# Kernel optimization log

Hardware: AMD Instinct MI355X
Metric: run time of the kernel (lower is better)

## Reference

```python
import jax, jax.numpy as jnp
import numpy as np

B, K, T, D, NH, HD, DFF, L = 2, 512, 2048, 1024, 16, 64, 4096, 2
EPS = 1e-5


def rotate_half(x):
    x1, x2 = jnp.split(x, 2, axis=-1)
    return jnp.concatenate([-x2, x1], axis=-1)


def rmsnorm(x, w):
    return x * jax.lax.rsqrt(jnp.mean(x * x, axis=-1, keepdims=True) + EPS) * w


def setup_inputs():
    key = jax.random.key(0)
    ks = jax.random.split(key, 16)
    x_processed = jax.random.normal(ks[0], (B, K, D), jnp.float32)
    # counts[b] = number of chunks n; boundaries[b, :n-1] = ascending chunk ends in (0, T),
    # positions >= n-1 padded with T (sentinel, never used by the original loop).
    counts = jax.random.randint(ks[1], (B,), K // 2, K + 1)
    raw = jnp.sort(jax.random.randint(ks[2], (B, K), 1, T), axis=1)
    j = jnp.arange(K)[None, :]
    boundaries = jnp.where(j < counts[:, None] - 1, raw, T)
    x_residual = jax.random.normal(ks[3], (B, T, D), jnp.float32)
    inv_freq = 1.0 / (10000.0 ** (jnp.arange(0, HD, 2, dtype=jnp.float32) / HD))
    freqs = jnp.arange(T, dtype=jnp.float32)[:, None] * inv_freq[None, :]  # [T, HD//2]
    emb = jnp.concatenate([freqs, freqs], axis=-1)                          # [T, HD]
    cos, sin = jnp.cos(emb), jnp.sin(emb)
    s = 0.02
    wq = jax.random.normal(ks[4], (L, D, D), jnp.float32) * s
    wk = jax.random.normal(ks[5], (L, D, D), jnp.float32) * s
    wv = jax.random.normal(ks[6], (L, D, D), jnp.float32) * s
    wo = jax.random.normal(ks[7], (L, D, D), jnp.float32) * s
    w1 = jax.random.normal(ks[8], (L, D, DFF), jnp.float32) * s
    w3 = jax.random.normal(ks[9], (L, D, DFF), jnp.float32) * s
    w2 = jax.random.normal(ks[10], (L, DFF, D), jnp.float32) * s
    attn_norm_w = jnp.ones((L, D), jnp.float32)
    mlp_norm_w = jnp.ones((L, D), jnp.float32)
    final_norm_w = jnp.ones((D,), jnp.float32)
    return {"x_processed": x_processed, "boundaries": boundaries, "counts": counts,
            "x_residual": x_residual, "cos": cos, "sin": sin, "seq_len": T,
            "wq": wq, "wk": wk, "wv": wv, "wo": wo,
            "attn_norm_w": attn_norm_w, "mlp_norm_w": mlp_norm_w,
            "w1": w1, "w3": w3, "w2": w2, "final_norm_w": final_norm_w}


def reference(x_processed, boundaries, counts, x_residual, cos, sin, seq_len,
              wq, wk, wv, wo, attn_norm_w, mlp_norm_w, w1, w3, w2, final_norm_w):
    Bn, Kn, Dn = x_processed.shape
    Tn = x_residual.shape[1]
    # Vectorized chunk expansion: token t belongs to chunk i = #{boundaries <= t}
    # (boundaries ascending; entries beyond n-1 are padded with seq_len so they never count).
    t = jnp.arange(Tn)
    idx = jax.vmap(lambda row: jnp.searchsorted(row, t, side='right'))(boundaries)  # [B, T]
    x = jnp.take_along_axis(x_processed, idx[:, :, None], axis=1) + x_residual     # [B, T, D]

    mask = jnp.tril(jnp.ones((Tn, Tn), dtype=bool))
    scale = 1.0 / jnp.sqrt(jnp.float32(HD))
    c = cos[None, :, None, :]
    s = sin[None, :, None, :]
    for l in range(L):
        h = rmsnorm(x, attn_norm_w[l])
        q = (h @ wq[l]).reshape(Bn, Tn, NH, HD)
        k = (h @ wk[l]).reshape(Bn, Tn, NH, HD)
        v = (h @ wv[l]).reshape(Bn, Tn, NH, HD)
        q = q * c + rotate_half(q) * s
        k = k * c + rotate_half(k) * s
        scores = jnp.einsum('bthd,bshd->bhts', q, k) * scale
        scores = jnp.where(mask[None, None], scores, -jnp.inf)
        probs = jax.nn.softmax(scores, axis=-1)
        o = jnp.einsum('bhts,bshd->bthd', probs, v).reshape(Bn, Tn, Dn)
        x = x + o @ wo[l]
        h = rmsnorm(x, mlp_norm_w[l])
        x = x + (jax.nn.silu(h @ w1[l]) * (h @ w3[l])) @ w2[l]
    return rmsnorm(x, final_norm_w)
```

## Files before the change

### kernel.cpp

```cpp
#include <hip/hip_runtime.h>
#include <stdint.h>

typedef __attribute__((ext_vector_type(8))) short s16x8;
typedef __attribute__((ext_vector_type(4))) float f32x4;

#define CB 2
#define CT 2048
#define CD 1024
#define CNH 16
#define CHD 64
#define CDFF 4096
#define CKB 512

__device__ __forceinline__ short f2bf(float f){
  union { float f; uint32_t u; } v; v.f = f;
  uint32_t r = v.u + 0x7FFFu + ((v.u >> 16) & 1u);
  return (short)(r >> 16);
}
__device__ __forceinline__ float bf2f(short h){
  union { uint32_t u; float f; } v; v.u = ((uint32_t)(uint16_t)h) << 16;
  return v.f;
}
__device__ __forceinline__ uint32_t cvtpk_bf16(float lo, float hi){
  uint32_t r;
  asm("v_cvt_pk_bf16_f32 %0, %1, %2" : "=v"(r) : "v"(lo), "v"(hi));
  return r;
}

#define GLOAD16(g, l) __builtin_amdgcn_global_load_lds( \
    (const __attribute__((address_space(1))) void*)(g), \
    (__attribute__((address_space(3))) void*)(l), 16, 0, 0)

__global__ void gather_rms_kernel(const float* __restrict__ xp, const int* __restrict__ bnd,
                                  const float* __restrict__ xr, const float* __restrict__ w,
                                  float* __restrict__ x, short* __restrict__ hbuf){
  int row = blockIdx.x;
  int b = row >> 11, t = row & 2047;
  int tid = threadIdx.x;
  int lo = 0, hi = CKB;
  while (lo < hi){ int mid = (lo + hi) >> 1; if (bnd[b*CKB + mid] <= t) lo = mid + 1; else hi = mid; }
  const float4 s  = ((const float4*)(xp + ((size_t)b*CKB + lo)*CD))[tid];
  const float4 rr = ((const float4*)(xr + (size_t)row*CD))[tid];
  float4 a; a.x = s.x + rr.x; a.y = s.y + rr.y; a.z = s.z + rr.z; a.w = s.w + rr.w;
  ((float4*)(x + (size_t)row*CD))[tid] = a;
  float ss = a.x*a.x + a.y*a.y + a.z*a.z + a.w*a.w;
  #pragma unroll
  for (int m = 1; m < 64; m <<= 1) ss += __shfl_xor(ss, m);
  __shared__ float red[4];
  if ((tid & 63) == 0) red[tid >> 6] = ss;
  __syncthreads();
  float tot = red[0] + red[1] + red[2] + red[3];
  float scale = rsqrtf(tot * (1.0f/1024.0f) + 1e-5f);
  const float4 wv = ((const float4*)w)[tid];
  short4 o;
  o.x = f2bf(a.x*scale*wv.x); o.y = f2bf(a.y*scale*wv.y);
  o.z = f2bf(a.z*scale*wv.z); o.w = f2bf(a.w*scale*wv.w);
  ((short4*)hbuf)[(size_t)row*256 + tid] = o;
}

__global__ void wtrans_qkvo_kernel(const float* __restrict__ wq, const float* __restrict__ wk,
                                   const float* __restrict__ wv, const float* __restrict__ wo,
                                   short* __restrict__ qkvT, short* __restrict__ woT){
  __shared__ __align__(16) float tile[64*65];
  const float* W; short* dst;
  const int z = blockIdx.z;
  if (z == 0){ W = wq; dst = qkvT; }
  else if (z == 1){ W = wk; dst = qkvT + (size_t)1024*1024; }
  else if (z == 2){ W = wv; dst = qkvT + (size_t)2048*1024; }
  else { W = wo; dst = woT; }
  int n0 = blockIdx.x*64, k0 = blockIdx.y*64;
  #pragma unroll
  for (int i = 0; i < 16; ++i){
    int e = threadIdx.x + 256*i; int kl = e >> 6, nl = e & 63;
    tile[kl*65 + nl] = W[(size_t)(k0 + kl)*1024 + n0 + nl];
  }
  __syncthreads();
  #pragma unroll
  for (int i = 0; i < 16; ++i){
    int e = threadIdx.x + 256*i; int nl = e >> 6, kl = e & 63;
    dst[(size_t)(n0 + nl)*1024 + k0 + kl] = f2bf(tile[kl*65 + nl]);
  }
}

__global__ void wtrans_kernel(const float* __restrict__ W, short* __restrict__ dst,
                              int Kd, int Nd){
  __shared__ __align__(16) float tile[64*65];
  int n0 = blockIdx.x*64, k0 = blockIdx.y*64;
  #pragma unroll
  for (int i = 0; i < 16; ++i){
    int e = threadIdx.x + 256*i; int kl = e >> 6, nl = e & 63;
    tile[kl*65 + nl] = W[(size_t)(k0 + kl)*Nd + n0 + nl];
  }
  __syncthreads();
  #pragma unroll
  for (int i = 0; i < 16; ++i){
    int e = threadIdx.x + 256*i; int nl = e >> 6, kl = e & 63;
    dst[(size_t)(n0 + nl)*Kd + k0 + kl] = f2bf(tile[kl*65 + nl]);
  }
}

__global__ void wtrans_inter2_kernel(const float* __restrict__ w1p, const float* __restrict__ w3p,
                                     short* __restrict__ dst){
  __shared__ __align__(16) float tile[64*65];
  const float* W = blockIdx.z ? w3p : w1p;
  const int off16 = blockIdx.z ? 16 : 0;
  int n0 = blockIdx.x*64, k0 = blockIdx.y*64;
  #pragma unroll
  for (int i = 0; i < 16; ++i){
    int e = threadIdx.x + 256*i; int kl = e >> 6, nl = e & 63;
    tile[kl*65 + nl] = W[(size_t)(k0 + kl)*4096 + n0 + nl];
  }
  __syncthreads();
  #pragma unroll
  for (int i = 0; i < 16; ++i){
    int e = threadIdx.x + 256*i; int nl = e >> 6, kl = e & 63;
    int c = n0 + nl;
    int frow = ((c >> 4) << 5) + off16 + (c & 15);
    dst[(size_t)frow*1024 + k0 + kl] = f2bf(tile[kl*65 + nl]);
  }
}

template<int OUT_BF16>
__global__ void redrms_kernel(float* __restrict__ x, const short* __restrict__ Cp,
                              const float* __restrict__ w, void* __restrict__ outv){
  int row = blockIdx.x, tid = threadIdx.x;
  size_t i = (size_t)row*256 + tid;
  const short4* p0 = (const short4*)Cp;
  const short4* p1 = p0 + (size_t)1048576;
  const short4* p2 = p1 + (size_t)1048576;
  const short4* p3 = p2 + (size_t)1048576;
  float4 a = ((float4*)x)[i];
  short4 q0 = p0[i], q1 = p1[i], q2 = p2[i], q3 = p3[i];
  a.x += (bf2f(q0.x) + bf2f(q1.x)) + (bf2f(q2.x) + bf2f(q3.x));
  a.y += (bf2f(q0.y) + bf2f(q1.y)) + (bf2f(q2.y) + bf2f(q3.y));
  a.z += (bf2f(q0.z) + bf2f(q1.z)) + (bf2f(q2.z) + bf2f(q3.z));
  a.w += (bf2f(q0.w) + bf2f(q1.w)) + (bf2f(q2.w) + bf2f(q3.w));
  if (OUT_BF16) ((float4*)x)[i] = a;
  float ss = a.x*a.x + a.y*a.y + a.z*a.z + a.w*a.w;
  #pragma unroll
  for (int m = 1; m < 64; m <<= 1) ss += __shfl_xor(ss, m);
  __shared__ float red[4];
  if ((tid & 63) == 0) red[tid >> 6] = ss;
  __syncthreads();
  float tot = red[0] + red[1] + red[2] + red[3];
  float scale = rsqrtf(tot * (1.0f/1024.0f) + 1e-5f);
  const float4 wv = ((const float4*)w)[tid];
  if (OUT_BF16){
    short4 o;
    o.x = f2bf(a.x*scale*wv.x); o.y = f2bf(a.y*scale*wv.y);
    o.z = f2bf(a.z*scale*wv.z); o.w = f2bf(a.w*scale*wv.w);
    ((short4*)outv)[(size_t)row*256 + tid] = o;
  } else {
    float4 o;
    o.x = a.x*scale*wv.x; o.y = a.y*scale*wv.y;
    o.z = a.z*scale*wv.z; o.w = a.w*scale*wv.w;
    ((float4*)outv)[(size_t)row*256 + tid] = o;
  }
}

__device__ __forceinline__ void swz_block_id(int id, int NX, int NY, int& bm, int& bn){
  const int nwg = NX*NY;
  const int qq = nwg >> 3, rr8 = nwg & 7;
  const int xcd = id & 7, loc = id >> 3;
  const int wgid = (xcd < rr8 ? xcd*(qq+1) : rr8*(qq+1) + (xcd-rr8)*qq) + loc;
  const int GM = 8;
  const int gsz = GM * NX;
  const int gidg = wgid / gsz;
  const int remg = wgid - gidg*gsz;
  bm = gidg*GM + (remg % GM);
  bn = remg / GM;
}

__global__ __launch_bounds__(256) void gemm_splitk(const short* __restrict__ A,
                                                   const short* __restrict__ Bt,
                                                   short* __restrict__ Cp,
                                                   int M, int N, int Ktot, int Kchunk,
                                                   int NX, int NY){
  __shared__ __align__(16) short sA[2][128*32];
  __shared__ __align__(16) short sB[2][128*32];
  const int tid = threadIdx.x;
  const int lane = tid & 63, wid = tid >> 6;
  const int wm = wid >> 1, wn = wid & 1;
  const int lr = lane & 15, lg = lane >> 4;
  const int nin = NX*NY;
  const int split = blockIdx.x / nin;
  const int inner = blockIdx.x - split*nin;
  int bm, bn; swz_block_id(inner, NX, NY, bm, bn);
  const int bm0 = bm * 128, bn0 = bn * 128;
  const int koff = split * Kchunk;

  f32x4 acc[4][4];
  #pragma unroll
  for (int i = 0; i < 4; ++i)
    #pragma unroll
    for (int j = 0; j < 4; ++j) acc[i][j] = (f32x4){0.f,0.f,0.f,0.f};

  const short* gA = A  + (size_t)(bm0 + wid*32 + (lane >> 2))*Ktot + koff + (lane & 3)*8;
  const short* gB = Bt + (size_t)(bn0 + wid*32 + (lane >> 2))*Ktot + koff + (lane & 3)*8;

  #pragma unroll
  for (int iss = 0; iss < 2; ++iss){
    GLOAD16(gA + (size_t)iss*16*Ktot, &sA[0][wid*1024 + iss*16*32]);
    GLOAD16(gB + (size_t)iss*16*Ktot, &sB[0][wid*1024 + iss*16*32]);
  }
  __syncthreads();

  int cur = 0;
  for (int k0 = 0; k0 < Kchunk; k0 += 32){
    if (k0 + 32 < Kchunk){
      #pragma unroll
      for (int iss = 0; iss < 2; ++iss){
        GLOAD16(gA + (size_t)iss*16*Ktot + k0 + 32, &sA[cur^1][wid*1024 + iss*16*32]);
        GLOAD16(gB + (size_t)iss*16*Ktot + k0 + 32, &sB[cur^1][wid*1024 + iss*16*32]);
      }
    }
    s16x8 af[4], bq[4];
    #pragma unroll
    for (int i = 0; i < 4; ++i) af[i] = *(const s16x8*)&sA[cur][(wm*64 + i*16 + lr)*32 + lg*8];
    #pragma unroll
    for (int j = 0; j < 4; ++j) bq[j] = *(const s16x8*)&sB[cur][(wn*64 + j*16 + lr)*32 + lg*8];
    #pragma unroll
    for (int i = 0; i < 4; ++i)
      #pragma unroll
      for (int j = 0; j < 4; ++j)
        acc[i][j] = __builtin_amdgcn_mfma_f32_16x16x32_bf16(af[i], bq[j], acc[i][j], 0, 0, 0);
    __syncthreads();
    cur ^= 1;
  }

  short* C = Cp + (size_t)split*M*N;
  #pragma unroll
  for (int i = 0; i < 4; ++i){
    int row0 = bm0 + wm*64 + i*16 + lg*4;
    #pragma unroll
    for (int j = 0; j < 4; ++j){
      int col = bn0 + wn*64 + j*16 + lr;
      #pragma unroll
      for (int r = 0; r < 4; ++r) C[(size_t)(row0 + r)*N + col] = f2bf(acc[i][j][r]);
    }
  }
}

#define STAGE8(u, kt, bufx) do { \
  const short* Gp_ = ((u)&1) ? Bt : A; \
  const int rb_ = ((u)&1) ? bn0 : bm0; \
  const int kh_ = (u)>>1; \
  _Pragma("unroll") \
  for (int L_ = 0; L_ < 2; ++L_){ \
    int rowS_ = L_*128 + wid*16 + (lane>>2); \
    int sp_ = (lane&3) ^ ((rowS_>>1)&3); \
    GLOAD16(Gp_ + (size_t)(rb_ + rowS_)*Kstr + (size_t)(kt)*64 + kh_*32 + sp_*8, \
            &sAB[bufx][u][(L_*512 + wid*64)*8]); \
  } \
} while(0)

#define LDSRD(bufx, u, rowv) \
  (*(const s16x8*)&sAB[bufx][u][(rowv)*32 + (((lg) ^ (((rowv)>>1)&3))<<3)])

template<int FUSE>
__global__ __launch_bounds__(512, 2) void gemm8p(const short* __restrict__ A,
                                                 const short* __restrict__ Bt,
                                                 void* __restrict__ Cv,
                                                 short* __restrict__ Qo,
                                                 short* __restrict__ Ko,
                                                 short* __restrict__ Vo,
                                                 const float* __restrict__ cosb,
                                                 const float* __restrict__ sinb,
                                                 int M, int N, int Kstr, int Kchunk,
                                                 int NX, int NY){
  __shared__ __align__(16) short sAB[2][4][256*32];
  const int tid = threadIdx.x;
  const int lane = tid & 63, wid = tid >> 6;
  const int wm = wid >> 2, wn = wid & 3;
  const int lr = lane & 15, lg = lane >> 4;
  const int nin = NX*NY;
  const int split = blockIdx.x / nin;
  const int inner = blockIdx.x - split*nin;
  int bm, bn; swz_block_id(inner, NX, NY, bm, bn);
  const int bm0 = bm * 256, bn0 = bn * 256;
  A  += (size_t)split * Kchunk;
  Bt += (size_t)split * Kchunk;

  f32x4 acc[8][4];
  #pragma unroll
  for (int i = 0; i < 8; ++i)
    #pragma unroll
    for (int j = 0; j < 4; ++j) acc[i][j] = (f32x4){0.f,0.f,0.f,0.f};

  const int NK = Kchunk >> 6;
  STAGE8(0, 0, 0); STAGE8(1, 0, 0); STAGE8(2, 0, 0); STAGE8(3, 0, 0);
  if (NK > 1){
    STAGE8(0, 1, 1); STAGE8(1, 1, 1); STAGE8(2, 1, 1);
    asm volatile("s_waitcnt vmcnt(10)" ::: "memory");
  } else {
    asm volatile("s_waitcnt vmcnt(4)" ::: "memory");
  }
  __builtin_amdgcn_s_barrier();

  s16x8 afp[8];
  #pragma unroll 1
  for (int kt = 0; kt < NK; ++kt){
    const int cur = kt & 1, nxt = cur ^ 1;
    const bool st1 = (kt + 1 < NK);
    const bool st2 = (kt + 2 < NK);

    if (st1) STAGE8(3, kt+1, nxt);
    {
      #pragma unroll
      for (int i_ = 0; i_ < 8; ++i_) afp[i_] = LDSRD(cur, 0, wm*128 + i_*16 + lr);
      s16x8 b0 = LDSRD(cur, 1, wn*64 + lr);
      s16x8 b1 = LDSRD(cur, 1, wn*64 + 16 + lr);
      __builtin_amdgcn_s_barrier();
      asm volatile("s_waitcnt lgkmcnt(0)" ::: "memory");
      __builtin_amdgcn_s_setprio(1);
      #pragma unroll
      for (int i_ = 0; i_ < 8; ++i_){
        acc[i_][0] = __builtin_amdgcn_mfma_f32_16x16x32_bf16(afp[i_], b0, acc[i_][0], 0, 0, 0);
        acc[i_][1] = __builtin_amdgcn_mfma_f32_16x16x32_bf16(afp[i_], b1, acc[i_][1], 0, 0, 0);
      }
      __builtin_amdgcn_s_setprio(0);
      __builtin_amdgcn_s_barrier();
    }
    if (st2) STAGE8(0, kt+2, cur);
    {
      s16x8 b2 = LDSRD(cur, 1, wn*64 + 32 + lr);
      s16x8 b3 = LDSRD(cur, 1, wn*64 + 48 + lr);
      __builtin_amdgcn_s_barrier();
      asm volatile("s_waitcnt lgkmcnt(0)" ::: "memory");
      __builtin_amdgcn_s_setprio(1);
      #pragma unroll
      for (int i_ = 0; i_ < 8; ++i_){
        acc[i_][2] = __builtin_amdgcn_mfma_f32_16x16x32_bf16(afp[i_], b2, acc[i_][2], 0, 0, 0);
        acc[i_][3] = __builtin_amdgcn_mfma_f32_16x16x32_bf16(afp[i_], b3, acc[i_][3], 0, 0, 0);
      }
      __builtin_amdgcn_s_setprio(0);
      if (st2)      asm volatile("s_waitcnt vmcnt(10)" ::: "memory");
      else if (st1) asm volatile("s_waitcnt vmcnt(8)"  ::: "memory");
      else          asm volatile("s_waitcnt vmcnt(0)"  ::: "memory");
      __builtin_amdgcn_s_barrier();
    }
    if (st2) STAGE8(1, kt+2, cur);
    {
      #pragma unroll
      for (int i_ = 0; i_ < 8; ++i_) afp[i_] = LDSRD(cur, 2, wm*128 + i_*16 + lr);
      s16x8 b0 = LDSRD(cur, 3, wn*64 + lr);
      s16x8 b1 = LDSRD(cur, 3, wn*64 + 16 + lr);
      __builtin_amdgcn_s_barrier();
      asm volatile("s_waitcnt lgkmcnt(0)" ::: "memory");
      __builtin_amdgcn_s_setprio(1);
      #pragma unroll
      for (int i_ = 0; i_ < 8; ++i_){
        acc[i_][0] = __builtin_amdgcn_mfma_f32_16x16x32_bf16(afp[i_], b0, acc[i_][0], 0, 0, 0);
        acc[i_][1] = __builtin_amdgcn_mfma_f32_16x16x32_bf16(afp[i_], b1, acc[i_][1], 0, 0, 0);
      }
      __builtin_amdgcn_s_setprio(0);
      __builtin_amdgcn_s_barrier();
    }
    if (st2) STAGE8(2, kt+2, cur);
    {
      s16x8 b2 = LDSRD(cur, 3, wn*64 + 32 + lr);
      s16x8 b3 = LDSRD(cur, 3, wn*64 + 48 + lr);
      __builtin_amdgcn_s_barrier();
      asm volatile("s_waitcnt lgkmcnt(0)" ::: "memory");
      __builtin_amdgcn_s_setprio(1);
      #pragma unroll
      for (int i_ = 0; i_ < 8; ++i_){
        acc[i_][2] = __builtin_amdgcn_mfma_f32_16x16x32_bf16(afp[i_], b2, acc[i_][2], 0, 0, 0);
        acc[i_][3] = __builtin_amdgcn_mfma_f32_16x16x32_bf16(afp[i_], b3, acc[i_][3], 0, 0, 0);
      }
      __builtin_amdgcn_s_setprio(0);
      if (st2)      asm volatile("s_waitcnt vmcnt(10)" ::: "memory");
      else if (st1) asm volatile("s_waitcnt vmcnt(4)"  ::: "memory");
      __builtin_amdgcn_s_barrier();
    }
  }

  if (FUSE == 0){
    short* C = (short*)Cv;
    #pragma unroll
    for (int i = 0; i < 8; ++i){
      int row0 = bm0 + wm*128 + i*16 + lg*4;
      #pragma unroll
      for (int j = 0; j < 4; ++j){
        int col = bn0 + wn*64 + j*16 + lr;
        #pragma unroll
        for (int r = 0; r < 4; ++r) C[(size_t)(row0 + r)*N + col] = f2bf(acc[i][j][r]);
      }
    }
  } else if (FUSE == 1){
    short* C = (short*)Cv;
    const int Nh = N >> 1;
    #pragma unroll
    for (int i = 0; i < 8; ++i){
      int row0 = bm0 + wm*128 + i*16 + lg*4;
      #pragma unroll
      for (int jp = 0; jp < 2; ++jp){
        int col = (bn0 >> 1) + wn*32 + jp*16 + lr;
        #pragma unroll
        for (int r = 0; r < 4; ++r){
          float u = acc[i][jp*2][r], g = acc[i][jp*2+1][r];
          float val = u / (1.f + __expf(-u)) * g;
          C[(size_t)(row0 + r)*Nh + col] = f2bf(val);
        }
      }
    }
  } else if (FUSE == 2){
    short* C = (short*)Cv + (size_t)split*M*N;
    #pragma unroll
    for (int i = 0; i < 8; ++i){
      int row0 = bm0 + wm*128 + i*16 + lg*4;
      #pragma unroll
      for (int j = 0; j < 4; ++j){
        int col = bn0 + wn*64 + j*16 + lr;
        #pragma unroll
        for (int r = 0; r < 4; ++r) C[(size_t)(row0 + r)*N + col] = f2bf(acc[i][j][r]);
      }
    }
  } else {
    const int part = bn0 >> 10;
    const int colb = bn0 & 1023;
    const int h = (colb + wn*64) >> 6;
    if (part < 2){
      short* dst = (part == 0) ? Qo : Ko;
      const float qs = (part == 0) ? 0.1803368801111204f : 1.0f;
      #pragma unroll
      for (int i = 0; i < 8; ++i){
        int row0 = bm0 + wm*128 + i*16 + lg*4;
        #pragma unroll
        for (int jh = 0; jh < 2; ++jh){
          int d = jh*16 + lr;
          #pragma unroll
          for (int r = 0; r < 4; ++r){
            int tg = row0 + r;
            int bb = tg >> 11, tt = tg & 2047;
            float c = cosb[tt*64 + d], s = sinb[tt*64 + d];
            float x0 = acc[i][jh][r], x1 = acc[i][jh+2][r];
            float y0 = (x0*c - x1*s)*qs;
            float y1 = (x1*c + x0*s)*qs;
            size_t o = ((size_t)(bb*CT + tt)*CNH + h)*CHD;
            dst[o + d]      = f2bf(y0);
            dst[o + d + 32] = f2bf(y1);
          }
        }
      }
    } else {
      #pragma unroll
      for (int i = 0; i < 8; ++i){
        int row0 = bm0 + wm*128 + i*16 + lg*4;
        int bb = row0 >> 11, t0 = row0 & 2047;
        #pragma unroll
        for (int j = 0; j < 4; ++j){
          int d = j*16 + lr;
          short4 pk;
          pk.x = f2bf(acc[i][j][0]); pk.y = f2bf(acc[i][j][1]);
          pk.z = f2bf(acc[i][j][2]); pk.w = f2bf(acc[i][j][3]);
          *(short4*)&Vo[((size_t)(bb*CNH + h)*CHD + d)*CT + t0] = pk;
        }
      }
    }
  }
}

__global__ __launch_bounds__(256) void attn_kernel(const short* __restrict__ Q,
                                                   const short* __restrict__ Kb,
                                                   const short* __restrict__ Vt,
                                                   short* __restrict__ O){
  __shared__ __align__(16) short Kl[2][64*72];
  __shared__ __align__(16) short Vl[2][64*72];
  __shared__ __align__(16) short Pl[4][16*72];
  const int tid = threadIdx.x, lane = tid & 63, w = tid >> 6;
  const int qpair = blockIdx.x;
  const int h = blockIdx.y, b = blockIdx.z;
  const int lr = lane & 15, lg = lane >> 4;

  const short* gK = Kb + (size_t)b*CT*CD + h*CHD;
  const short* gV = Vt + (size_t)(b*CNH + h)*CHD*CT;
  const int srow0 = tid >> 3, scol = (tid & 7)*8;

  #pragma unroll 1
  for (int half = 0; half < 2; ++half){
    const int qt = half ? qpair : (31 - qpair);
    const int wq0 = qt*64 + w*16;
    const int jmax = qt + 1;

    s16x8 qf0, qf1;
    {
      const short* qp = Q + ((size_t)(b*CT + wq0 + lr)*CNH + h)*CHD + lg*8;
      qf0 = *(const s16x8*)qp;
      qf1 = *(const s16x8*)(qp + 32);
    }
    f32x4 oacc[4];
    #pragma unroll
    for (int dt = 0; dt < 4; ++dt) oacc[dt] = (f32x4){0.f,0.f,0.f,0.f};
    float m_r = -1e30f, l_r = 0.f;

    #pragma unroll
    for (int p = 0; p < 2; ++p){
      int row = srow0 + p*32;
      *(s16x8*)&Kl[0][row*72 + scol] = *(const s16x8*)(gK + (size_t)row*CD + scol);
      *(s16x8*)&Vl[0][row*72 + scol] = *(const s16x8*)(gV + (size_t)row*CT + scol);
    }
    __syncthreads();

    #pragma unroll 1
    for (int j = 0; j < jmax; ++j){
      const int kv0 = j*64;
      const int buf = j & 1;
      s16x8 nk[2], nv[2];
      const bool havenext = (j + 1 < jmax);
      if (havenext){
        const int kv1 = kv0 + 64;
        #pragma unroll
        for (int p = 0; p < 2; ++p){
          int row = srow0 + p*32;
          nk[p] = *(const s16x8*)(gK + (size_t)(kv1 + row)*CD + scol);
          nv[p] = *(const s16x8*)(gV + (size_t)row*CT + kv1 + scol);
        }
      }

      if (kv0 < wq0 + 16){
        f32x4 sc[4];
        __builtin_amdgcn_s_setprio(1);
        #pragma unroll
        for (int nt = 0; nt < 4; ++nt){
          s16x8 k0 = *(const s16x8*)&Kl[buf][(nt*16 + lr)*72 + lg*8];
          s16x8 k1 = *(const s16x8*)&Kl[buf][(nt*16 + lr)*72 + 32 + lg*8];
          f32x4 z = (f32x4){0.f,0.f,0.f,0.f};
          z = __builtin_amdgcn_mfma_f32_16x16x32_bf16(k0, qf0, z, 0, 0, 0);
          z = __builtin_amdgcn_mfma_f32_16x16x32_bf16(k1, qf1, z, 0, 0, 0);
          sc[nt] = z;
        }
        __builtin_amdgcn_s_setprio(0);
        if (kv0 + 64 > wq0){
          #pragma unroll
          for (int nt = 0; nt < 4; ++nt)
            #pragma unroll
            for (int r = 0; r < 4; ++r)
              if (kv0 + nt*16 + lg*4 + r > wq0 + lr) sc[nt][r] = -1e30f;
        }
        float pmax = sc[0][0];
        #pragma unroll
        for (int nt = 0; nt < 4; ++nt)
          #pragma unroll
          for (int r = 0; r < 4; ++r) pmax = fmaxf(pmax, sc[nt][r]);
        pmax = fmaxf(pmax, __shfl_xor(pmax, 16));
        pmax = fmaxf(pmax, __shfl_xor(pmax, 32));
        if (!__all(pmax - m_r <= 10.f)){
          float mn = fmaxf(m_r, pmax);
          float corr = __builtin_amdgcn_exp2f(m_r - mn);
          m_r = mn;
          l_r *= corr;
          #pragma unroll
          for (int r = 0; r < 4; ++r){
            float c4 = __shfl(corr, lg*4 + r);
            #pragma unroll
            for (int dt = 0; dt < 4; ++dt) oacc[dt][r] *= c4;
          }
        }
        float rs = 0.f;
        #pragma unroll
        for (int nt = 0; nt < 4; ++nt)
          #pragma unroll
          for (int r = 0; r < 4; ++r){
            float pv = __builtin_amdgcn_exp2f(sc[nt][r] - m_r);
            sc[nt][r] = pv;
            rs += pv;
          }
        #pragma unroll
        for (int nt = 0; nt < 4; ++nt){
          uint2 pk;
          pk.x = cvtpk_bf16(sc[nt][0], sc[nt][1]);
          pk.y = cvtpk_bf16(sc[nt][2], sc[nt][3]);
          *(uint2*)&Pl[w][lr*72 + nt*16 + lg*4] = pk;
        }
        rs += __shfl_xor(rs, 16);
        rs += __shfl_xor(rs, 32);
        l_r += rs;
        s16x8 pa0 = *(const s16x8*)&Pl[w][lr*72 + lg*8];
        s16x8 pa1 = *(const s16x8*)&Pl[w][lr*72 + 32 + lg*8];
        __builtin_amdgcn_s_setprio(1);
        #pragma unroll
        for (int dt = 0; dt < 4; ++dt){
          s16x8 v0 = *(const s16x8*)&Vl[buf][(dt*16 + lr)*72 + lg*8];
          s16x8 v1 = *(const s16x8*)&Vl[buf][(dt*16 + lr)*72 + 32 + lg*8];
          oacc[dt] = __builtin_amdgcn_mfma_f32_16x16x32_bf16(pa0, v0, oacc[dt], 0, 0, 0);
          oacc[dt] = __builtin_amdgcn_mfma_f32_16x16x32_bf16(pa1, v1, oacc[dt], 0, 0, 0);
        }
        __builtin_amdgcn_s_setprio(0);
      }
      if (havenext){
        #pragma unroll
        for (int p = 0; p < 2; ++p){
          int row = srow0 + p*32;
          *(s16x8*)&Kl[buf^1][row*72 + scol] = nk[p];
          *(s16x8*)&Vl[buf^1][row*72 + scol] = nv[p];
        }
      }
      __syncthreads();
    }

    #pragma unroll
    for (int r = 0; r < 4; ++r){
      float lf = __shfl(l_r, lg*4 + r);
      float inv = 1.f / lf;
      int qrow = wq0 + lg*4 + r;
      #pragma unroll
      for (int dt = 0; dt < 4; ++dt)
        O[((size_t)(b*CT + qrow)*CNH + h)*CHD + dt*16 + lr] = f2bf(oacc[dt][r] * inv);
    }
  }
}

extern "C" void kernel_launch(void* const* d_in, const int* in_sizes, int n_in,
                              void* d_out, int out_size, void* d_ws, size_t ws_size,
                              hipStream_t stream){
  (void)in_sizes; (void)n_in; (void)out_size; (void)ws_size;
  const float* x_processed = (const float*)d_in[0];
  const int*   boundaries  = (const int*)d_in[1];
  const float* x_residual  = (const float*)d_in[3];
  const float* cosb        = (const float*)d_in[4];
  const float* sinb        = (const float*)d_in[5];
  const float* wq          = (const float*)d_in[7];
  const float* wk          = (const float*)d_in[8];
  const float* wv          = (const float*)d_in[9];
  const float* wo          = (const float*)d_in[10];
  const float* attn_nw     = (const float*)d_in[11];
  const float* mlp_nw      = (const float*)d_in[12];
  const float* w1          = (const float*)d_in[13];
  const float* w3          = (const float*)d_in[14];
  const float* w2          = (const float*)d_in[15];
  const float* final_nw    = (const float*)d_in[16];

  char* p = (char*)d_ws;
  auto alloc = [&](size_t bytes)->char*{
    char* r = p; p += (bytes + 255) & ~(size_t)255; return r;
  };
  short* wqkvT = (short*)alloc((size_t)2*3072*1024*2);
  short* woT   = (short*)alloc((size_t)2*1024*1024*2);
  short* w13T  = (short*)alloc((size_t)2*8192*1024*2);
  short* w2T   = (short*)alloc((size_t)2*1024*4096*2);
  float* x     = (float*)alloc((size_t)4096*1024*4);
  short* hbuf  = (short*)alloc((size_t)4096*1024*2);
  short* qr    = (short*)alloc((size_t)4096*1024*2);
  short* kr    = (short*)alloc((size_t)4096*1024*2);
  short* vt    = (short*)alloc((size_t)4096*1024*2);
  short* obuf  = (short*)alloc((size_t)4096*1024*2);
  short* mbuf  = (short*)alloc((size_t)4096*4096*2);
  short* psum  = (short*)alloc((size_t)4*4096*1024*2);

  for (int l = 0; l < 2; ++l){
    size_t wOff = (size_t)l*1024*1024;
    wtrans_qkvo_kernel<<<dim3(16,16,4),256,0,stream>>>(wq + wOff, wk + wOff, wv + wOff, wo + wOff,
                                                       wqkvT + (size_t)l*3072*1024, woT + (size_t)l*1024*1024);
    wtrans_inter2_kernel<<<dim3(64,16,2),256,0,stream>>>(w1 + (size_t)l*1024*4096, w3 + (size_t)l*1024*4096,
                                                         w13T + (size_t)l*8192*1024);
    wtrans_kernel<<<dim3(16,64),256,0,stream>>>(w2 + (size_t)l*4096*1024, w2T + (size_t)l*1024*4096, 4096, 1024);
  }
  gather_rms_kernel<<<4096,256,0,stream>>>(x_processed, boundaries, x_residual, attn_nw, x, hbuf);
  for (int l = 0; l < 2; ++l){
    gemm8p<3><<<12*16,512,0,stream>>>(hbuf, wqkvT + (size_t)l*3072*1024, nullptr,
                                      qr, kr, vt, cosb, sinb,
                                      4096, 3072, 1024, 1024, 12, 16);
    attn_kernel<<<dim3(16,16,2),256,0,stream>>>(qr, kr, vt, obuf);
    gemm_splitk<<<8*32*4,256,0,stream>>>(obuf, woT + (size_t)l*1024*1024, psum,
                                         4096, 1024, 1024, 256, 8, 32);
    redrms_kernel<1><<<4096,256,0,stream>>>(x, psum, mlp_nw + l*1024, hbuf);
    gemm8p<1><<<32*16,512,0,stream>>>(hbuf, w13T + (size_t)l*8192*1024, mbuf,
                                      nullptr, nullptr, nullptr, nullptr, nullptr,
                                      4096, 8192, 1024, 1024, 32, 16);
    gemm8p<2><<<4*4*16,512,0,stream>>>(mbuf, w2T + (size_t)l*1024*4096, psum,
                                       nullptr, nullptr, nullptr, nullptr, nullptr,
                                       4096, 1024, 4096, 1024, 4, 16);
    if (l == 0) redrms_kernel<1><<<4096,256,0,stream>>>(x, psum, attn_nw + 1024, hbuf);
    else        redrms_kernel<0><<<4096,256,0,stream>>>(x, psum, final_nw, d_out);
  }
}
```

Measured before the change: 551.0 us.

## Split attention into one q-tile per block and deepen W2 split-K

The attention kernel previously had each block process a pair of query tiles (qt and 31-qt) in sequence. It now launches 1024 blocks, each handling one query tile, with a head/batch-interleaved mapping that pairs long and short tiles across neighbouring blocks. Separately, the down-projection GEMM now splits K into 8 partial slices of 512 instead of 4 of 1024, and the reduce+RMSNorm kernel is templated on the number of partial sums. Both changes aim to raise parallelism and balance work across CUs, at the cost of a larger partial-sum buffer and more reduction traffic.

```diff
diff --git a/kernel.cpp b/kernel.cpp
--- a/kernel.cpp
+++ b/kernel.cpp
@@ -120,21 +120,17 @@
   }
 }
 
-template<int OUT_BF16>
+template<int OUT_BF16, int NS>
 __global__ void redrms_kernel(float* __restrict__ x, const short* __restrict__ Cp,
                               const float* __restrict__ w, void* __restrict__ outv){
   int row = blockIdx.x, tid = threadIdx.x;
   size_t i = (size_t)row*256 + tid;
-  const short4* p0 = (const short4*)Cp;
-  const short4* p1 = p0 + (size_t)1048576;
-  const short4* p2 = p1 + (size_t)1048576;
-  const short4* p3 = p2 + (size_t)1048576;
   float4 a = ((float4*)x)[i];
-  short4 q0 = p0[i], q1 = p1[i], q2 = p2[i], q3 = p3[i];
-  a.x += (bf2f(q0.x) + bf2f(q1.x)) + (bf2f(q2.x) + bf2f(q3.x));
-  a.y += (bf2f(q0.y) + bf2f(q1.y)) + (bf2f(q2.y) + bf2f(q3.y));
-  a.z += (bf2f(q0.z) + bf2f(q1.z)) + (bf2f(q2.z) + bf2f(q3.z));
-  a.w += (bf2f(q0.w) + bf2f(q1.w)) + (bf2f(q2.w) + bf2f(q3.w));
+  #pragma unroll
+  for (int s = 0; s < NS; ++s){
+    short4 q = ((const short4*)Cp)[(size_t)s*1048576 + i];
+    a.x += bf2f(q.x); a.y += bf2f(q.y); a.z += bf2f(q.z); a.w += bf2f(q.w);
+  }
   if (OUT_BF16) ((float4*)x)[i] = a;
   float ss = a.x*a.x + a.y*a.y + a.z*a.z + a.w*a.w;
   #pragma unroll
@@ -469,145 +465,151 @@
   __shared__ __align__(16) short Vl[2][64*72];
   __shared__ __align__(16) short Pl[4][16*72];
   const int tid = threadIdx.x, lane = tid & 63, w = tid >> 6;
-  const int qpair = blockIdx.x;
-  const int h = blockIdx.y, b = blockIdx.z;
+  const int id = blockIdx.x;
+  const int hlo = id & 7;
+  const int rest = id >> 3;
+  const int c = rest & 31;
+  const int hb = rest >> 5;
+  const int hhi = hb & 1, b = hb >> 1;
+  int qt;
+  if (hb == 0)      qt = c;
+  else if (hb == 1) qt = 31 - c;
+  else if (hb == 2) qt = (c + 16) & 31;
+  else              qt = 31 - ((c + 16) & 31);
+  const int h = (hhi << 3) | hlo;
   const int lr = lane & 15, lg = lane >> 4;
 
   const short* gK = Kb + (size_t)b*CT*CD + h*CHD;
   const short* gV = Vt + (size_t)(b*CNH + h)*CHD*CT;
   const int srow0 = tid >> 3, scol = (tid & 7)*8;
 
+  const int wq0 = qt*64 + w*16;
+  const int jmax = qt + 1;
+
+  s16x8 qf0, qf1;
+  {
+    const short* qp = Q + ((size_t)(b*CT + wq0 + lr)*CNH + h)*CHD + lg*8;
+    qf0 = *(const s16x8*)qp;
+    qf1 = *(const s16x8*)(qp + 32);
+  }
+  f32x4 oacc[4];
+  #pragma unroll
+  for (int dt = 0; dt < 4; ++dt) oacc[dt] = (f32x4){0.f,0.f,0.f,0.f};
+  float m_r = -1e30f, l_r = 0.f;
+
+  #pragma unroll
+  for (int p = 0; p < 2; ++p){
+    int row = srow0 + p*32;
+    *(s16x8*)&Kl[0][row*72 + scol] = *(const s16x8*)(gK + (size_t)row*CD + scol);
+    *(s16x8*)&Vl[0][row*72 + scol] = *(const s16x8*)(gV + (size_t)row*CT + scol);
+  }
+  __syncthreads();
+
   #pragma unroll 1
-  for (int half = 0; half < 2; ++half){
-    const int qt = half ? qpair : (31 - qpair);
-    const int wq0 = qt*64 + w*16;
-    const int jmax = qt + 1;
-
-    s16x8 qf0, qf1;
-    {
-      const short* qp = Q + ((size_t)(b*CT + wq0 + lr)*CNH + h)*CHD + lg*8;
-      qf0 = *(const s16x8*)qp;
-      qf1 = *(const s16x8*)(qp + 32);
-    }
-    f32x4 oacc[4];
-    #pragma unroll
-    for (int dt = 0; dt < 4; ++dt) oacc[dt] = (f32x4){0.f,0.f,0.f,0.f};
-    float m_r = -1e30f, l_r = 0.f;
-
-    #pragma unroll
-    for (int p = 0; p < 2; ++p){
-      int row = srow0 + p*32;
-      *(s16x8*)&Kl[0][row*72 + scol] = *(const s16x8*)(gK + (size_t)row*CD + scol);
-      *(s16x8*)&Vl[0][row*72 + scol] = *(const s16x8*)(gV + (size_t)row*CT + scol);
-    }
-    __syncthreads();
-
-    #pragma unroll 1
-    for (int j = 0; j < jmax; ++j){
-      const int kv0 = j*64;
-      const int buf = j & 1;
-      s16x8 nk[2], nv[2];
-      const bool havenext = (j + 1 < jmax);
-      if (havenext){
-        const int kv1 = kv0 + 64;
-        #pragma unroll
-        for (int p = 0; p < 2; ++p){
-          int row = srow0 + p*32;
-          nk[p] = *(const s16x8*)(gK + (size_t)(kv1 + row)*CD + scol);
-          nv[p] = *(const s16x8*)(gV + (size_t)row*CT + kv1 + scol);
-        }
-      }
-
-      if (kv0 < wq0 + 16){
-        f32x4 sc[4];
-        __builtin_amdgcn_s_setprio(1);
-        #pragma unroll
-        for (int nt = 0; nt < 4; ++nt){
-          s16x8 k0 = *(const s16x8*)&Kl[buf][(nt*16 + lr)*72 + lg*8];
-          s16x8 k1 = *(const s16x8*)&Kl[buf][(nt*16 + lr)*72 + 32 + lg*8];
-          f32x4 z = (f32x4){0.f,0.f,0.f,0.f};
-          z = __builtin_amdgcn_mfma_f32_16x16x32_bf16(k0, qf0, z, 0, 0, 0);
-          z = __builtin_amdgcn_mfma_f32_16x16x32_bf16(k1, qf1, z, 0, 0, 0);
-          sc[nt] = z;
-        }
-        __builtin_amdgcn_s_setprio(0);
-        if (kv0 + 64 > wq0){
-          #pragma unroll
-          for (int nt = 0; nt < 4; ++nt)
-            #pragma unroll
-            for (int r = 0; r < 4; ++r)
-              if (kv0 + nt*16 + lg*4 + r > wq0 + lr) sc[nt][r] = -1e30f;
-        }
-        float pmax = sc[0][0];
+  for (int j = 0; j < jmax; ++j){
+    const int kv0 = j*64;
+    const int buf = j & 1;
+    s16x8 nk[2], nv[2];
+    const bool havenext = (j + 1 < jmax);
+    if (havenext){
+      const int kv1 = kv0 + 64;
+      #pragma unroll
+      for (int p = 0; p < 2; ++p){
+        int row = srow0 + p*32;
+        nk[p] = *(const s16x8*)(gK + (size_t)(kv1 + row)*CD + scol);
+        nv[p] = *(const s16x8*)(gV + (size_t)row*CT + kv1 + scol);
+      }
+    }
+
+    if (kv0 < wq0 + 16){
+      f32x4 sc[4];
+      __builtin_amdgcn_s_setprio(1);
+      #pragma unroll
+      for (int nt = 0; nt < 4; ++nt){
+        s16x8 k0 = *(const s16x8*)&Kl[buf][(nt*16 + lr)*72 + lg*8];
+        s16x8 k1 = *(const s16x8*)&Kl[buf][(nt*16 + lr)*72 + 32 + lg*8];
+        f32x4 z = (f32x4){0.f,0.f,0.f,0.f};
+        z = __builtin_amdgcn_mfma_f32_16x16x32_bf16(k0, qf0, z, 0, 0, 0);
+        z = __builtin_amdgcn_mfma_f32_16x16x32_bf16(k1, qf1, z, 0, 0, 0);
+        sc[nt] = z;
+      }
+      __builtin_amdgcn_s_setprio(0);
+      if (kv0 + 64 > wq0){
         #pragma unroll
         for (int nt = 0; nt < 4; ++nt)
           #pragma unroll
-          for (int r = 0; r < 4; ++r) pmax = fmaxf(pmax, sc[nt][r]);
-        pmax = fmaxf(pmax, __shfl_xor(pmax, 16));
-        pmax = fmaxf(pmax, __shfl_xor(pmax, 32));
-        if (!__all(pmax - m_r <= 10.f)){
-          float mn = fmaxf(m_r, pmax);
-          float corr = __builtin_amdgcn_exp2f(m_r - mn);
-          m_r = mn;
-          l_r *= corr;
+          for (int r = 0; r < 4; ++r)
+            if (kv0 + nt*16 + lg*4 + r > wq0 + lr) sc[nt][r] = -1e30f;
+      }
+      float pmax = sc[0][0];
+      #pragma unroll
+      for (int nt = 0; nt < 4; ++nt)
+        #pragma unroll
+        for (int r = 0; r < 4; ++r) pmax = fmaxf(pmax, sc[nt][r]);
+      pmax = fmaxf(pmax, __shfl_xor(pmax, 16));
+      pmax = fmaxf(pmax, __shfl_xor(pmax, 32));
+      if (!__all(pmax - m_r <= 10.f)){
+        float mn = fmaxf(m_r, pmax);
+        float corr = __builtin_amdgcn_exp2f(m_r - mn);
+        m_r = mn;
+        l_r *= corr;
+        #pragma unroll
+        for (int r = 0; r < 4; ++r){
+          float c4 = __shfl(corr, lg*4 + r);
           #pragma unroll
-          for (int r = 0; r < 4; ++r){
-            float c4 = __shfl(corr, lg*4 + r);
-            #pragma unroll
-            for (int dt = 0; dt < 4; ++dt) oacc[dt][r] *= c4;
-          }
+          for (int dt = 0; dt < 4; ++dt) oacc[dt][r] *= c4;
         }
-        float rs = 0.f;
-        #pragma unroll
-        for (int nt = 0; nt < 4; ++nt)
-          #pragma unroll
-          for (int r = 0; r < 4; ++r){
-            float pv = __builtin_amdgcn_exp2f(sc[nt][r] - m_r);
-            sc[nt][r] = pv;
-            rs += pv;
-          }
-        #pragma unroll
-        for (int nt = 0; nt < 4; ++nt){
-          uint2 pk;
-          pk.x = cvtpk_bf16(sc[nt][0], sc[nt][1]);
-          pk.y = cvtpk_bf16(sc[nt][2], sc[nt][3]);
-          *(uint2*)&Pl[w][lr*72 + nt*16 + lg*4] = pk;
+      }
+      float rs = 0.f;
+      #pragma unroll
+      for (int nt = 0; nt < 4; ++nt)
+        #pragma unroll
+        for (int r = 0; r < 4; ++r){
+          float pv = __builtin_amdgcn_exp2f(sc[nt][r] - m_r);
+          sc[nt][r] = pv;
+          rs += pv;
         }
-        rs += __shfl_xor(rs, 16);
-        rs += __shfl_xor(rs, 32);
-        l_r += rs;
-        s16x8 pa0 = *(const s16x8*)&Pl[w][lr*72 + lg*8];
-        s16x8 pa1 = *(const s16x8*)&Pl[w][lr*72 + 32 + lg*8];
-        __builtin_amdgcn_s_setprio(1);
-        #pragma unroll
-        for (int dt = 0; dt < 4; ++dt){
-          s16x8 v0 = *(const s16x8*)&Vl[buf][(dt*16 + lr)*72 + lg*8];
-          s16x8 v1 = *(const s16x8*)&Vl[buf][(dt*16 + lr)*72 + 32 + lg*8];
-          oacc[dt] = __builtin_amdgcn_mfma_f32_16x16x32_bf16(pa0, v0, oacc[dt], 0, 0, 0);
-          oacc[dt] = __builtin_amdgcn_mfma_f32_16x16x32_bf16(pa1, v1, oacc[dt], 0, 0, 0);
-        }
-        __builtin_amdgcn_s_setprio(0);
-      }
-      if (havenext){
-        #pragma unroll
-        for (int p = 0; p < 2; ++p){
-          int row = srow0 + p*32;
-          *(s16x8*)&Kl[buf^1][row*72 + scol] = nk[p];
-          *(s16x8*)&Vl[buf^1][row*72 + scol] = nv[p];
-        }
-      }
-      __syncthreads();
-    }
-
-    #pragma unroll
-    for (int r = 0; r < 4; ++r){
-      float lf = __shfl(l_r, lg*4 + r);
-      float inv = 1.f / lf;
-      int qrow = wq0 + lg*4 + r;
-      #pragma unroll
-      for (int dt = 0; dt < 4; ++dt)
-        O[((size_t)(b*CT + qrow)*CNH + h)*CHD + dt*16 + lr] = f2bf(oacc[dt][r] * inv);
-    }
+      #pragma unroll
+      for (int nt = 0; nt < 4; ++nt){
+        uint2 pk;
+        pk.x = cvtpk_bf16(sc[nt][0], sc[nt][1]);
+        pk.y = cvtpk_bf16(sc[nt][2], sc[nt][3]);
+        *(uint2*)&Pl[w][lr*72 + nt*16 + lg*4] = pk;
+      }
+      rs += __shfl_xor(rs, 16);
+      rs += __shfl_xor(rs, 32);
+      l_r += rs;
+      s16x8 pa0 = *(const s16x8*)&Pl[w][lr*72 + lg*8];
+      s16x8 pa1 = *(const s16x8*)&Pl[w][lr*72 + 32 + lg*8];
+      __builtin_amdgcn_s_setprio(1);
+      #pragma unroll
+      for (int dt = 0; dt < 4; ++dt){
+        s16x8 v0 = *(const s16x8*)&Vl[buf][(dt*16 + lr)*72 + lg*8];
+        s16x8 v1 = *(const s16x8*)&Vl[buf][(dt*16 + lr)*72 + 32 + lg*8];
+        oacc[dt] = __builtin_amdgcn_mfma_f32_16x16x32_bf16(pa0, v0, oacc[dt], 0, 0, 0);
+        oacc[dt] = __builtin_amdgcn_mfma_f32_16x16x32_bf16(pa1, v1, oacc[dt], 0, 0, 0);
+      }
+      __builtin_amdgcn_s_setprio(0);
+    }
+    if (havenext){
+      #pragma unroll
+      for (int p = 0; p < 2; ++p){
+        int row = srow0 + p*32;
+        *(s16x8*)&Kl[buf^1][row*72 + scol] = nk[p];
+        *(s16x8*)&Vl[buf^1][row*72 + scol] = nv[p];
+      }
+    }
+    __syncthreads();
+  }
+
+  #pragma unroll
+  for (int r = 0; r < 4; ++r){
+    float lf = __shfl(l_r, lg*4 + r);
+    float inv = 1.f / lf;
+    int qrow = wq0 + lg*4 + r;
+    #pragma unroll
+    for (int dt = 0; dt < 4; ++dt)
+      O[((size_t)(b*CT + qrow)*CNH + h)*CHD + dt*16 + lr] = f2bf(oacc[dt][r] * inv);
   }
 }
 
@@ -646,7 +648,7 @@
   short* vt    = (short*)alloc((size_t)4096*1024*2);
   short* obuf  = (short*)alloc((size_t)4096*1024*2);
   short* mbuf  = (short*)alloc((size_t)4096*4096*2);
-  short* psum  = (short*)alloc((size_t)4*4096*1024*2);
+  short* psum  = (short*)alloc((size_t)8*4096*1024*2);
 
   for (int l = 0; l < 2; ++l){
     size_t wOff = (size_t)l*1024*1024;
@@ -661,17 +663,17 @@
     gemm8p<3><<<12*16,512,0,stream>>>(hbuf, wqkvT + (size_t)l*3072*1024, nullptr,
                                       qr, kr, vt, cosb, sinb,
                                       4096, 3072, 1024, 1024, 12, 16);
-    attn_kernel<<<dim3(16,16,2),256,0,stream>>>(qr, kr, vt, obuf);
+    attn_kernel<<<1024,256,0,stream>>>(qr, kr, vt, obuf);
     gemm_splitk<<<8*32*4,256,0,stream>>>(obuf, woT + (size_t)l*1024*1024, psum,
                                          4096, 1024, 1024, 256, 8, 32);
-    redrms_kernel<1><<<4096,256,0,stream>>>(x, psum, mlp_nw + l*1024, hbuf);
+    redrms_kernel<1,4><<<4096,256,0,stream>>>(x, psum, mlp_nw + l*1024, hbuf);
     gemm8p<1><<<32*16,512,0,stream>>>(hbuf, w13T + (size_t)l*8192*1024, mbuf,
                                       nullptr, nullptr, nullptr, nullptr, nullptr,
                                       4096, 8192, 1024, 1024, 32, 16);
-    gemm8p<2><<<4*4*16,512,0,stream>>>(mbuf, w2T + (size_t)l*1024*4096, psum,
+    gemm8p<2><<<8*4*16,512,0,stream>>>(mbuf, w2T + (size_t)l*1024*4096, psum,
                                        nullptr, nullptr, nullptr, nullptr, nullptr,
-                                       4096, 1024, 4096, 1024, 4, 16);
-    if (l == 0) redrms_kernel<1><<<4096,256,0,stream>>>(x, psum, attn_nw + 1024, hbuf);
-    else        redrms_kernel<0><<<4096,256,0,stream>>>(x, psum, final_nw, d_out);
-  }
-}
+                                       4096, 1024, 4096, 512, 4, 16);
+    if (l == 0) redrms_kernel<1,8><<<4096,256,0,stream>>>(x, psum, attn_nw + 1024, hbuf);
+    else        redrms_kernel<0,8><<<4096,256,0,stream>>>(x, psum, final_nw, d_out);
+  }
+}
```

Result: slower. 598.4 us (+8.6%).
